# Kernel optimization log

Measured on AMD Instinct MI355X. Metric: run time of the kernel, lower is better.

Reference implementation:

```python
import jax, jax.numpy as jnp
import numpy as np

K, D, B = 2048, 50257, 256
N_CLASS = 2

def setup_inputs() -> dict:
    key = jax.random.key(0)
    k1, k2, k3 = jax.random.split(key, 3)
    # strictly positive (probability-like) entries so log() is finite
    queue_anchor = jax.random.uniform(k1, (K, D), dtype=jnp.float32, minval=1e-3, maxval=1.0)
    query = jax.random.uniform(k2, (B, D), dtype=jnp.float32, minval=1e-3, maxval=1.0)
    queue_label = jax.random.randint(k3, (K,), 0, N_CLASS, dtype=jnp.int64)
    return {"query": query, "queue_anchor": queue_anchor, "queue_label": queue_label}

def reference(query, queue_anchor, queue_label):
    # torch code: mean_d( a[:,None,:] * (log a[:,None,:] - log q) ).T  -> [B, K]
    # algebraically identical, avoiding the (K,B,D) intermediate:
    #   kl[b,k] = mean_d(a_k * log a_k) - (1/D) * sum_d a_k[d] * log q_b[d]
    d = queue_anchor.shape[1]
    self_term = jnp.mean(queue_anchor * jnp.log(queue_anchor), axis=1)        # [K]
    cross_term = jnp.einsum('kd,bd->kb', queue_anchor, jnp.log(query)) / d    # [K, B]
    kl_distance = (self_term[:, None] - cross_term).T                          # [B, K]
    # knn == 1 path: nearest anchor's label per query
    return queue_label[jnp.argmin(kl_distance, axis=1)]                        # [B]
```

## Files before the change

### kernel.cpp

```cpp
#include <hip/hip_runtime.h>


constexpr int K    = 2048;
constexpr int D    = 50257;
constexpr int B    = 256;
constexpr int BM   = 32;
constexpr int BK   = 64;
constexpr int DSPL = 25344;
constexpr int LQS  = 25408;
constexpr int NC   = 8;
constexpr float MARGIN = 4.0f;

typedef __attribute__((ext_vector_type(8))) short bf16x8;
typedef __attribute__((ext_vector_type(4))) float f32x4;
typedef __attribute__((ext_vector_type(8))) unsigned short u16x8;

__device__ inline unsigned short f2bf_rne(float f) {
    union { float f; unsigned u; } v; v.f = f;
    unsigned r = v.u + 0x7FFFu + ((v.u >> 16) & 1u);
    return (unsigned short)(r >> 16);
}

__global__ __launch_bounds__(256)
void lq_kernel(const float* __restrict__ q, unsigned short* __restrict__ lq,
               int aoff, int DL)
{
    const int stride = gridDim.x * blockDim.x;
    const int total  = B * (LQS / 8);
    for (int c = blockIdx.x * blockDim.x + threadIdx.x; c < total; c += stride) {
        const int b  = c / (LQS / 8);
        const int o8 = (c % (LQS / 8)) * 8;
        u16x8 w;
#pragma unroll
        for (int j = 0; j < 8; ++j) {
            const int d = o8 + j;
            const float v = (d < DL) ? q[(size_t)b * D + aoff + d] : 1.f;
            w[j] = f2bf_rne(__logf(v));
        }
        *reinterpret_cast<u16x8*>(&lq[(size_t)b * LQS + o8]) = w;
    }
}

__global__ __launch_bounds__(512, 2)
void gemm_kernel(const float* __restrict__ anchor,
                 const unsigned short* __restrict__ lq,
                 float* __restrict__ part,
                 float* __restrict__ selfp,
                 int dc, int DL, int aoff, int zoff)
{
    const int nb8 = gridDim.x >> 3;
    const int g   = (blockIdx.x & 7) * nb8 + (blockIdx.x >> 3);
    const int z   = g >> 6;
    const int x   = g & 63;

    const int t    = threadIdx.x;
    const int k0   = x * BM;
    const int d0   = z * dc;
    const int DLr  = (DL + 63) & ~63;
    const int dend = min(d0 + dc, DLr);

    __shared__ __align__(16) unsigned short lds[(BM + B) * 64];

    const int rowA = t >> 4;
    const int cA   = (t & 15) * 4;
    const int ar   = k0 + rowA;
    const int swA  = (rowA & 7) << 3;
    const float* Arow = anchor + (size_t)ar * D + aoff;

    const int rowQ = t >> 1;
    const int hq   = (t & 1) * 32;
    const int swQ  = (rowQ & 7) << 3;
    const unsigned short* LQrow = lq + (size_t)rowQ * LQS;

    const int w    = t >> 6;
    const int lane = t & 63;
    const int wn   = w * 32;
    const int lrow = lane & 15;
    const int kg   = lane >> 4;

    f32x4 acc[2][2];
#pragma unroll
    for (int mt = 0; mt < 2; ++mt)
#pragma unroll
        for (int nt = 0; nt < 2; ++nt)
#pragma unroll
            for (int i = 0; i < 4; ++i) acc[mt][nt][i] = 0.f;

    float selfacc = 0.f;

    float wf[8]; int ph = 0;
    u16x8 qreg[4];

    auto load_step = [&](int dt) {
        const int dbase = dt + cA;
        if (dbase + 8 <= DL) {
            const size_t g0 = (size_t)ar * D + aoff + dbase;
            ph = (int)(g0 & 3);
            const float4* wp = reinterpret_cast<const float4*>(anchor + (g0 - ph));
            const float4 w0 = wp[0], w1 = wp[1];
            wf[0] = w0.x; wf[1] = w0.y; wf[2] = w0.z; wf[3] = w0.w;
            wf[4] = w1.x; wf[5] = w1.y; wf[6] = w1.z; wf[7] = w1.w;
        } else {
            ph = 0;
#pragma unroll
            for (int j = 0; j < 4; ++j) {
                const int d = dbase + j;
                wf[j] = (d < DL) ? Arow[d] : 0.f;
            }
#pragma unroll
            for (int j = 4; j < 8; ++j) wf[j] = 0.f;
        }
        const int qb = dt + hq;
#pragma unroll
        for (int gg = 0; gg < 4; ++gg)
            qreg[gg] = *reinterpret_cast<const u16x8*>(&LQrow[qb + 8 * gg]);
    };

    auto convert_write = [&]() {
        float s5[5], av[4];
#pragma unroll
        for (int j = 0; j < 5; ++j) s5[j] = (ph & 2) ? wf[j + 2] : wf[j];
#pragma unroll
        for (int j = 0; j < 4; ++j) av[j] = (ph & 1) ? s5[j + 1] : s5[j];
        ushort4 abf;
        {
            float a0 = av[0], a1 = av[1], a2 = av[2], a3 = av[3];
            if (a0 > 0.f) selfacc = fmaf(a0, __logf(a0), selfacc);
            if (a1 > 0.f) selfacc = fmaf(a1, __logf(a1), selfacc);
            if (a2 > 0.f) selfacc = fmaf(a2, __logf(a2), selfacc);
            if (a3 > 0.f) selfacc = fmaf(a3, __logf(a3), selfacc);
            abf = ushort4{f2bf_rne(a0), f2bf_rne(a1), f2bf_rne(a2), f2bf_rne(a3)};
        }
        *reinterpret_cast<ushort4*>(&lds[rowA * 64 + (cA ^ swA)]) = abf;
#pragma unroll
        for (int gg = 0; gg < 4; ++gg)
            *reinterpret_cast<u16x8*>(&lds[(BM + rowQ) * 64 + ((hq + 8 * gg) ^ swQ)]) = qreg[gg];
    };

    auto mfma_phase = [&]() {
#pragma unroll
        for (int half = 0; half < 2; ++half) {
            const int dd = half * 32;
            bf16x8 af[2], qf[2];
#pragma unroll
            for (int mt = 0; mt < 2; ++mt) {
                const int r = mt * 16 + lrow;
                const int c = (dd + kg * 8) ^ ((r & 7) << 3);
                af[mt] = *reinterpret_cast<const bf16x8*>(&lds[r * 64 + c]);
            }
#pragma unroll
            for (int nt = 0; nt < 2; ++nt) {
                const int r = wn + nt * 16 + lrow;
                const int c = (dd + kg * 8) ^ ((r & 7) << 3);
                qf[nt] = *reinterpret_cast<const bf16x8*>(&lds[(BM + r) * 64 + c]);
            }
#pragma unroll
            for (int mt = 0; mt < 2; ++mt)
#pragma unroll
                for (int nt = 0; nt < 2; ++nt)
                    acc[mt][nt] = __builtin_amdgcn_mfma_f32_16x16x32_bf16(
                        af[mt], qf[nt], acc[mt][nt], 0, 0, 0);
        }
    };

    if (d0 < dend) {
        load_step(d0);
        for (int dt = d0; dt < dend; dt += BK) {
            convert_write();
            __syncthreads();
            if (dt + BK < dend) load_step(dt + BK);
            mfma_phase();
            __syncthreads();
        }
    }

#pragma unroll
    for (int mt = 0; mt < 2; ++mt)
#pragma unroll
        for (int nt = 0; nt < 2; ++nt) {
            const int kk = k0 + mt * 16 + kg * 4;
            const int bb = wn + nt * 16 + lrow;
            *reinterpret_cast<f32x4*>(&part[((size_t)z * B + bb) * K + kk]) = acc[mt][nt];
        }

    float s = selfacc;
    s += __shfl_xor(s, 1);
    s += __shfl_xor(s, 2);
    s += __shfl_xor(s, 4);
    s += __shfl_xor(s, 8);
    if ((t & 15) == 0) selfp[(size_t)(zoff + z) * K + ar] = s;
}

__global__ __launch_bounds__(256)
void reduce_kernel(const float* __restrict__ part, float* __restrict__ crossA, int pch)
{
    const int i = blockIdx.x * 256 + threadIdx.x;
    const f32x4* p4 = reinterpret_cast<const f32x4*>(part);
    f32x4 s = p4[i];
    for (int z = 1; z < pch; ++z) {
        const f32x4 v = p4[(size_t)z * (B * K / 4) + i];
#pragma unroll
        for (int j = 0; j < 4; ++j) s[j] += v[j];
    }
    reinterpret_cast<f32x4*>(crossA)[i] = s;
}

__global__ __launch_bounds__(256)
void selfsum_kernel(const float* __restrict__ selfp, float* __restrict__ selftot, int rows)
{
    const int k = blockIdx.x * 256 + threadIdx.x;
    float s = 0.f;
    for (int z = 0; z < rows; ++z) s += selfp[(size_t)z * K + k];
    selftot[k] = s;
}

__global__ __launch_bounds__(256)
void topk_kernel(const float* __restrict__ crossA, const float* __restrict__ part,
                 const float* __restrict__ selftot,
                 int* __restrict__ cand, int* __restrict__ need, int pch)
{
    const int b = blockIdx.x, t = threadIdx.x;
    float v[8];
#pragma unroll
    for (int i = 0; i < 8; ++i) {
        const int k = i * 256 + t;
        float cv = crossA[(size_t)b * K + k];
        for (int z = 0; z < pch; ++z) cv += part[((size_t)z * B + b) * K + k];
        v[i] = selftot[k] - cv;
    }
    __shared__ float sv[256];
    __shared__ int   si[256];
    __shared__ float topv[2];
    for (int r = 0; r < NC; ++r) {
        float bv = 3.4e38f; int bk = K;
#pragma unroll
        for (int i = 0; i < 8; ++i) {
            const int k = i * 256 + t;
            if (v[i] < bv) { bv = v[i]; bk = k; }
        }
        sv[t] = bv; si[t] = bk;
        __syncthreads();
        for (int off = 128; off > 0; off >>= 1) {
            if (t < off) {
                if (sv[t + off] < sv[t] || (sv[t + off] == sv[t] && si[t + off] < si[t])) {
                    sv[t] = sv[t + off]; si[t] = si[t + off];
                }
            }
            __syncthreads();
        }
        const int kwin = si[0];
        if ((kwin & 255) == t) v[kwin >> 8] = 3.4e38f;
        if (t == 0) {
            cand[b * NC + r] = kwin;
            if (r < 2) topv[r] = sv[0];
        }
        __syncthreads();
    }
    if (t == 0) need[b] = (topv[1] - topv[0] < MARGIN) ? 1 : 0;
}

__global__ __launch_bounds__(512)
void rescore_kernel(const float* __restrict__ query, const float* __restrict__ anchor,
                    const int* __restrict__ cand, const int* __restrict__ need,
                    double* __restrict__ pp)
{
    const int b = blockIdx.x, h = blockIdx.y, t = threadIdx.x;
    if (!need[b]) return;
    const int dlo = h * 25129;
    const int dhi = min(D, dlo + 25129);
    int ks[NC];
#pragma unroll
    for (int c = 0; c < NC; ++c) ks[c] = cand[b * NC + c];
    const float* qrow = query + (size_t)b * D;

    double a8[NC];
#pragma unroll
    for (int c = 0; c < NC; ++c) a8[c] = 0.0;

    for (int d = dlo + t; d < dhi; d += 512) {
        const double lqv = (double)logf(qrow[d]);
#pragma unroll
        for (int c = 0; c < NC; ++c)
            a8[c] = fma((double)anchor[(size_t)ks[c] * D + d], lqv, a8[c]);
    }

    __shared__ double red[512];
    for (int c = 0; c < NC; ++c) {
        red[t] = a8[c];
        __syncthreads();
        for (int off = 256; off > 0; off >>= 1) {
            if (t < off) red[t] += red[t + off];
            __syncthreads();
        }
        if (t == 0) pp[((size_t)b * 2 + h) * NC + c] = red[0];
        __syncthreads();
    }
}

__global__ __launch_bounds__(256)
void final_kernel(const double* __restrict__ pp, const float* __restrict__ selftot,
                  const int* __restrict__ cand, const int* __restrict__ need,
                  const int* __restrict__ label, int* __restrict__ out)
{
    const int b = threadIdx.x;
    if (!need[b]) { out[b] = label[cand[b * NC]]; return; }
    float best = 3.4e38f; int bk = K;
#pragma unroll
    for (int c = 0; c < NC; ++c) {
        const int k = cand[b * NC + c];
        const double cv = pp[((size_t)b * 2 + 0) * NC + c] + pp[((size_t)b * 2 + 1) * NC + c];
        const float sc = selftot[k] - (float)cv;
        if (sc < best || (sc == best && k < bk)) { best = sc; bk = k; }
    }
    out[b] = label[bk];
}

extern "C" void kernel_launch(void* const* d_in, const int* in_sizes, int n_in,
                              void* d_out, int out_size, void* d_ws, size_t ws_size,
                              hipStream_t stream)
{
    const float* query  = (const float*)d_in[0];
    const float* anchor = (const float*)d_in[1];
    const int*   label  = (const int*)d_in[2];
    int* out = (int*)d_out;

    size_t cur = 0;
    auto alloc = [&](size_t bytes) -> void* {
        cur = (cur + 255) & ~(size_t)255;
        void* p = (char*)d_ws + cur;
        cur += bytes;
        return p;
    };

    unsigned short* lq      = (unsigned short*)alloc((size_t)B * LQS * 2);
    float*          crossA  = (float*)alloc((size_t)B * K * 4);
    float*          selfp   = (float*)alloc((size_t)12 * K * 4);
    float*          selftot = (float*)alloc((size_t)K * 4);
    int*            cand    = (int*)alloc((size_t)B * NC * 4);
    int*            need    = (int*)alloc((size_t)B * 4);
    double*         pp      = (double*)alloc((size_t)B * 2 * NC * 8);
    const size_t fixed_end  = cur;

    int pch = 1;
    for (int s = 6; s >= 1; --s) {
        if (fixed_end + (size_t)s * B * K * 4 + 256 <= ws_size) { pch = s; break; }
    }
    float* part = (float*)alloc((size_t)pch * B * K * 4);

    const int DL1 = DSPL, DL2 = D - DSPL;
    const int dc1 = ((DL1 + pch - 1) / pch + 63) & ~63;
    const int dc2 = ((DL2 + pch - 1) / pch + 63) & ~63;

    lq_kernel<<<2048, 256, 0, stream>>>(query, lq, 0, DL1);
    gemm_kernel<<<64 * pch, 512, 0, stream>>>(anchor, lq, part, selfp, dc1, DL1, 0, 0);
    reduce_kernel<<<B * K / 4 / 256, 256, 0, stream>>>(part, crossA, pch);

    lq_kernel<<<2048, 256, 0, stream>>>(query, lq, DSPL, DL2);
    gemm_kernel<<<64 * pch, 512, 0, stream>>>(anchor, lq, part, selfp, dc2, DL2, DSPL, pch);

    selfsum_kernel<<<K / 256, 256, 0, stream>>>(selfp, selftot, 2 * pch);
    topk_kernel<<<B, 256, 0, stream>>>(crossA, part, selftot, cand, need, pch);
    rescore_kernel<<<dim3(B, 2), 512, 0, stream>>>(query, anchor, cand, need, pp);
    final_kernel<<<1, 256, 0, stream>>>(pp, selftot, cand, need, label, out);
}
```

Baseline: 630.0 us.

## Double-buffer LDS tiles with two-stage register prefetch in GEMM kernel

Replaces the single LDS buffer and two-barrier loop with a ping-pong LDS buffer and two register staging sets, so global loads for step s+2 and the LDS write for step s+1 overlap the MFMA work of step s. Only one lightweight barrier (lgkmcnt wait plus s_barrier) is issued per step. Anchor loading is also remapped so only half the threads load A, each handling 8 elements with three float4 loads and tail masking instead of a scalar fallback branch. The cost is double the LDS use and more registers, which may reduce occupancy under the 2-blocks-per-CU launch bound.

After: 764.0 us. +21.3%, slower.

```diff
diff --git a/kernel.cpp b/kernel.cpp
--- a/kernel.cpp
+++ b/kernel.cpp
@@ -58,14 +58,15 @@
     const int d0   = z * dc;
     const int DLr  = (DL + 63) & ~63;
     const int dend = min(d0 + dc, DLr);
-
-    __shared__ __align__(16) unsigned short lds[(BM + B) * 64];
-
-    const int rowA = t >> 4;
-    const int cA   = (t & 15) * 4;
-    const int ar   = k0 + rowA;
+    const size_t KD = (size_t)K * D;
+
+    __shared__ __align__(16) unsigned short lds[2][(BM + B) * 64];
+
+    const int rowA = t >> 3;
+    const int cA   = (t & 7) * 8;
+    const int ar   = k0 + (rowA & 31);
     const int swA  = (rowA & 7) << 3;
-    const float* Arow = anchor + (size_t)ar * D + aoff;
+    const bool doA = (t < 256);
 
     const int rowQ = t >> 1;
     const int hq   = (t & 1) * 32;
@@ -88,56 +89,54 @@
 
     float selfacc = 0.f;
 
-    float wf[8]; int ph = 0;
-    u16x8 qreg[4];
-
-    auto load_step = [&](int dt) {
-        const int dbase = dt + cA;
-        if (dbase + 8 <= DL) {
-            const size_t g0 = (size_t)ar * D + aoff + dbase;
+    float wfA0[12]; int phA0 = 0, dbA0 = 0; u16x8 q0[4];
+    float wfA1[12]; int phA1 = 0, dbA1 = 0; u16x8 q1[4];
+
+    auto ld4 = [&](size_t fi) -> float4 {
+        if (fi > KD - 4) fi = KD - 4;
+        return *reinterpret_cast<const float4*>(anchor + fi);
+    };
+
+    auto load_step = [&](int dt, float (&wf)[12], int& ph, int& db, u16x8 (&qr)[4]) {
+        if (doA) {
+            db = dt + cA;
+            const size_t g0 = (size_t)ar * D + aoff + db;
             ph = (int)(g0 & 3);
-            const float4* wp = reinterpret_cast<const float4*>(anchor + (g0 - ph));
-            const float4 w0 = wp[0], w1 = wp[1];
-            wf[0] = w0.x; wf[1] = w0.y; wf[2] = w0.z; wf[3] = w0.w;
-            wf[4] = w1.x; wf[5] = w1.y; wf[6] = w1.z; wf[7] = w1.w;
-        } else {
-            ph = 0;
-#pragma unroll
-            for (int j = 0; j < 4; ++j) {
-                const int d = dbase + j;
-                wf[j] = (d < DL) ? Arow[d] : 0.f;
-            }
-#pragma unroll
-            for (int j = 4; j < 8; ++j) wf[j] = 0.f;
+            const size_t b0 = g0 - ph;
+            const float4 v0 = ld4(b0), v1 = ld4(b0 + 4), v2 = ld4(b0 + 8);
+            wf[0] = v0.x; wf[1]  = v0.y; wf[2]  = v0.z; wf[3]  = v0.w;
+            wf[4] = v1.x; wf[5]  = v1.y; wf[6]  = v1.z; wf[7]  = v1.w;
+            wf[8] = v2.x; wf[9]  = v2.y; wf[10] = v2.z; wf[11] = v2.w;
         }
         const int qb = dt + hq;
 #pragma unroll
         for (int gg = 0; gg < 4; ++gg)
-            qreg[gg] = *reinterpret_cast<const u16x8*>(&LQrow[qb + 8 * gg]);
-    };
-
-    auto convert_write = [&]() {
-        float s5[5], av[4];
-#pragma unroll
-        for (int j = 0; j < 5; ++j) s5[j] = (ph & 2) ? wf[j + 2] : wf[j];
-#pragma unroll
-        for (int j = 0; j < 4; ++j) av[j] = (ph & 1) ? s5[j + 1] : s5[j];
-        ushort4 abf;
-        {
-            float a0 = av[0], a1 = av[1], a2 = av[2], a3 = av[3];
-            if (a0 > 0.f) selfacc = fmaf(a0, __logf(a0), selfacc);
-            if (a1 > 0.f) selfacc = fmaf(a1, __logf(a1), selfacc);
-            if (a2 > 0.f) selfacc = fmaf(a2, __logf(a2), selfacc);
-            if (a3 > 0.f) selfacc = fmaf(a3, __logf(a3), selfacc);
-            abf = ushort4{f2bf_rne(a0), f2bf_rne(a1), f2bf_rne(a2), f2bf_rne(a3)};
-        }
-        *reinterpret_cast<ushort4*>(&lds[rowA * 64 + (cA ^ swA)]) = abf;
+            qr[gg] = *reinterpret_cast<const u16x8*>(&LQrow[qb + 8 * gg]);
+    };
+
+    auto convert_write = [&](unsigned short* L, float (&wf)[12], int ph, int db,
+                             u16x8 (&qr)[4]) {
+        if (doA) {
+            float s9[9], av[8];
+#pragma unroll
+            for (int j = 0; j < 9; ++j) s9[j] = (ph & 2) ? wf[j + 2] : wf[j];
+#pragma unroll
+            for (int j = 0; j < 8; ++j) av[j] = (ph & 1) ? s9[j + 1] : s9[j];
+            u16x8 abf;
+#pragma unroll
+            for (int j = 0; j < 8; ++j) {
+                float a = (db + j < DL) ? av[j] : 0.f;
+                if (a > 0.f) selfacc = fmaf(a, __logf(a), selfacc);
+                abf[j] = (short)f2bf_rne(a);
+            }
+            *reinterpret_cast<u16x8*>(&L[rowA * 64 + (cA ^ swA)]) = abf;
+        }
 #pragma unroll
         for (int gg = 0; gg < 4; ++gg)
-            *reinterpret_cast<u16x8*>(&lds[(BM + rowQ) * 64 + ((hq + 8 * gg) ^ swQ)]) = qreg[gg];
-    };
-
-    auto mfma_phase = [&]() {
+            *reinterpret_cast<u16x8*>(&L[(BM + rowQ) * 64 + ((hq + 8 * gg) ^ swQ)]) = qr[gg];
+    };
+
+    auto mfma_phase = [&](const unsigned short* L) {
 #pragma unroll
         for (int half = 0; half < 2; ++half) {
             const int dd = half * 32;
@@ -146,13 +145,13 @@
             for (int mt = 0; mt < 2; ++mt) {
                 const int r = mt * 16 + lrow;
                 const int c = (dd + kg * 8) ^ ((r & 7) << 3);
-                af[mt] = *reinterpret_cast<const bf16x8*>(&lds[r * 64 + c]);
+                af[mt] = *reinterpret_cast<const bf16x8*>(&L[r * 64 + c]);
             }
 #pragma unroll
             for (int nt = 0; nt < 2; ++nt) {
                 const int r = wn + nt * 16 + lrow;
                 const int c = (dd + kg * 8) ^ ((r & 7) << 3);
-                qf[nt] = *reinterpret_cast<const bf16x8*>(&lds[(BM + r) * 64 + c]);
+                qf[nt] = *reinterpret_cast<const bf16x8*>(&L[(BM + r) * 64 + c]);
             }
 #pragma unroll
             for (int mt = 0; mt < 2; ++mt)
@@ -163,14 +162,37 @@
         }
     };
 
+    auto soft_barrier = [&]() {
+        asm volatile("s_waitcnt lgkmcnt(0)" ::: "memory");
+        __builtin_amdgcn_sched_barrier(0);
+        __builtin_amdgcn_s_barrier();
+        __builtin_amdgcn_sched_barrier(0);
+    };
+
     if (d0 < dend) {
-        load_step(d0);
-        for (int dt = d0; dt < dend; dt += BK) {
-            convert_write();
-            __syncthreads();
-            if (dt + BK < dend) load_step(dt + BK);
-            mfma_phase();
-            __syncthreads();
+        const int n = (dend - d0) >> 6;
+        load_step(d0, wfA0, phA0, dbA0, q0);
+        if (n > 1) load_step(d0 + BK, wfA1, phA1, dbA1, q1);
+        convert_write(lds[0], wfA0, phA0, dbA0, q0);
+        soft_barrier();
+        for (int s = 0; s < n; ++s) {
+            if ((s & 1) == 0) {
+                if (s + 2 < n) load_step(d0 + (s + 2) * BK, wfA0, phA0, dbA0, q0);
+                __builtin_amdgcn_sched_barrier(0);
+                mfma_phase(lds[0]);
+                if (s + 1 < n) {
+                    convert_write(lds[1], wfA1, phA1, dbA1, q1);
+                    soft_barrier();
+                }
+            } else {
+                if (s + 2 < n) load_step(d0 + (s + 2) * BK, wfA1, phA1, dbA1, q1);
+                __builtin_amdgcn_sched_barrier(0);
+                mfma_phase(lds[1]);
+                if (s + 1 < n) {
+                    convert_write(lds[0], wfA0, phA0, dbA0, q0);
+                    soft_barrier();
+                }
+            }
         }
     }
 
@@ -187,8 +209,7 @@
     s += __shfl_xor(s, 1);
     s += __shfl_xor(s, 2);
     s += __shfl_xor(s, 4);
-    s += __shfl_xor(s, 8);
-    if ((t & 15) == 0) selfp[(size_t)(zoff + z) * K + ar] = s;
+    if (doA && (t & 7) == 0) selfp[(size_t)(zoff + z) * K + ar] = s;
 }
 
 __global__ __launch_bounds__(256)
```

## Split D across waves with register-resident tiles and LDS reduction in GEMM

Applied to the files above, without the earlier changes.

Rewrites the GEMM kernel so each of 8 waves owns a disjoint slice of D and keeps a 32x256 accumulator tile in registers. Anchor rows are loaded and converted per lane straight into MFMA operands, and log-query fragments are read from a new chunk-major global layout instead of staging through LDS with per-step barriers. Per-wave partial sums are combined at the end through a large LDS reduction. This removes the two barriers per K-step and the LDS staging traffic, at the cost of heavy register pressure, a large LDS footprint that limits occupancy, and a change of split count from up to 6 to powers of two.

Measured after the change: 536.9 us (median of 2 runs). 1.17x faster.

```diff
diff --git a/kernel.cpp b/kernel.cpp
--- a/kernel.cpp
+++ b/kernel.cpp
@@ -4,10 +4,7 @@
 constexpr int K    = 2048;
 constexpr int D    = 50257;
 constexpr int B    = 256;
-constexpr int BM   = 32;
-constexpr int BK   = 64;
 constexpr int DSPL = 25344;
-constexpr int LQS  = 25408;
 constexpr int NC   = 8;
 constexpr float MARGIN = 4.0f;
 
@@ -23,172 +20,187 @@
 
 __global__ __launch_bounds__(256)
 void lq_kernel(const float* __restrict__ q, unsigned short* __restrict__ lq,
-               int aoff, int DL)
+               int aoff, int DL, int nch)
 {
     const int stride = gridDim.x * blockDim.x;
-    const int total  = B * (LQS / 8);
+    const int total  = nch * B * 4;
     for (int c = blockIdx.x * blockDim.x + threadIdx.x; c < total; c += stride) {
-        const int b  = c / (LQS / 8);
-        const int o8 = (c % (LQS / 8)) * 8;
+        const int sub = c & 3;
+        const int b   = (c >> 2) & 255;
+        const int ch  = c >> 10;
+        const int d0  = ch * 32 + sub * 8;
         u16x8 w;
 #pragma unroll
         for (int j = 0; j < 8; ++j) {
-            const int d = o8 + j;
+            const int d = d0 + j;
             const float v = (d < DL) ? q[(size_t)b * D + aoff + d] : 1.f;
             w[j] = f2bf_rne(__logf(v));
         }
-        *reinterpret_cast<u16x8*>(&lq[(size_t)b * LQS + o8]) = w;
-    }
-}
-
-__global__ __launch_bounds__(512, 2)
+        *reinterpret_cast<u16x8*>(&lq[((size_t)ch * B + b) * 32 + sub * 8]) = w;
+    }
+}
+
+__global__ __launch_bounds__(512)
 void gemm_kernel(const float* __restrict__ anchor,
                  const unsigned short* __restrict__ lq,
                  float* __restrict__ part,
                  float* __restrict__ selfp,
-                 int dc, int DL, int aoff, int zoff)
+                 int dc, int DL, int DCAP, int aoff, int zoff)
 {
     const int nb8 = gridDim.x >> 3;
     const int g   = (blockIdx.x & 7) * nb8 + (blockIdx.x >> 3);
     const int z   = g >> 6;
-    const int x   = g & 63;
+    const int kt  = g & 63;
+    const int k0  = kt * 32;
 
     const int t    = threadIdx.x;
-    const int k0   = x * BM;
-    const int d0   = z * dc;
-    const int DLr  = (DL + 63) & ~63;
-    const int dend = min(d0 + dc, DLr);
-
-    __shared__ __align__(16) unsigned short lds[(BM + B) * 64];
-
-    const int rowA = t >> 4;
-    const int cA   = (t & 15) * 4;
-    const int ar   = k0 + rowA;
-    const int swA  = (rowA & 7) << 3;
-    const float* Arow = anchor + (size_t)ar * D + aoff;
-
-    const int rowQ = t >> 1;
-    const int hq   = (t & 1) * 32;
-    const int swQ  = (rowQ & 7) << 3;
-    const unsigned short* LQrow = lq + (size_t)rowQ * LQS;
-
-    const int w    = t >> 6;
+    const int wid  = t >> 6;
     const int lane = t & 63;
-    const int wn   = w * 32;
-    const int lrow = lane & 15;
-    const int kg   = lane >> 4;
-
-    f32x4 acc[2][2];
-#pragma unroll
-    for (int mt = 0; mt < 2; ++mt)
-#pragma unroll
-        for (int nt = 0; nt < 2; ++nt)
-#pragma unroll
-            for (int i = 0; i < 4; ++i) acc[mt][nt][i] = 0.f;
-
-    float selfacc = 0.f;
-
-    float wf[8]; int ph = 0;
-    u16x8 qreg[4];
-
-    auto load_step = [&](int dt) {
-        const int dbase = dt + cA;
-        if (dbase + 8 <= DL) {
-            const size_t g0 = (size_t)ar * D + aoff + dbase;
-            ph = (int)(g0 & 3);
-            const float4* wp = reinterpret_cast<const float4*>(anchor + (g0 - ph));
-            const float4 w0 = wp[0], w1 = wp[1];
-            wf[0] = w0.x; wf[1] = w0.y; wf[2] = w0.z; wf[3] = w0.w;
-            wf[4] = w1.x; wf[5] = w1.y; wf[6] = w1.z; wf[7] = w1.w;
-        } else {
-            ph = 0;
-#pragma unroll
-            for (int j = 0; j < 4; ++j) {
-                const int d = dbase + j;
-                wf[j] = (d < DL) ? Arow[d] : 0.f;
+    const int lr   = lane & 15;
+    const int lg   = lane >> 4;
+
+    const int zd0 = z * dc;
+    const int zd1 = min(zd0 + dc, DCAP);
+    const int wd  = ((dc / 8) + 31) & ~31;
+    const int d0  = zd0 + wid * wd;
+    const int d1  = min(d0 + wd, zd1);
+
+    const size_t KDm4 = (size_t)K * D - 4;
+
+    f32x4 acc0[16], acc1[16];
+#pragma unroll
+    for (int j = 0; j < 16; ++j)
+#pragma unroll
+        for (int i = 0; i < 4; ++i) { acc0[j][i] = 0.f; acc1[j][i] = 0.f; }
+
+    float sacc0 = 0.f, sacc1 = 0.f;
+
+    if (d0 < d1) {
+        const int ar0 = k0 + lr;
+        const int ar1 = ar0 + 16;
+        const size_t gA0 = (size_t)ar0 * D + aoff + d0 + lg * 8;
+        const size_t gA1 = (size_t)ar1 * D + aoff + d0 + lg * 8;
+        const int ph0 = (int)(gA0 & 3);
+        const int ph1 = (int)(gA1 & 3);
+        size_t iA0 = gA0 - ph0;
+        size_t iA1 = gA1 - ph1;
+
+        const unsigned short* qp =
+            lq + ((size_t)(d0 >> 5) * (B * 32) + (size_t)lr * 32 + lg * 8);
+
+        auto ld4 = [&](size_t fi) -> float4 {
+            if (fi > KDm4) fi = KDm4;
+            return *reinterpret_cast<const float4*>(anchor + fi);
+        };
+
+        for (int dd = d0; dd < d1; dd += 32) {
+            const int dbase = dd + lg * 8;
+            bf16x8 af0, af1;
+            {
+                const float4 v0 = ld4(iA0), v1 = ld4(iA0 + 4), v2 = ld4(iA0 + 8);
+                float wf[12] = {v0.x, v0.y, v0.z, v0.w, v1.x, v1.y, v1.z, v1.w,
+                                v2.x, v2.y, v2.z, v2.w};
+                float s9[9];
+#pragma unroll
+                for (int j = 0; j < 9; ++j) s9[j] = (ph0 & 2) ? wf[j + 2] : wf[j];
+#pragma unroll
+                for (int j = 0; j < 8; ++j) {
+                    float a = (ph0 & 1) ? s9[j + 1] : s9[j];
+                    a = (dbase + j < DL) ? a : 0.f;
+                    if (a > 0.f) sacc0 = fmaf(a, __logf(a), sacc0);
+                    af0[j] = (short)f2bf_rne(a);
+                }
+                iA0 += 32;
             }
-#pragma unroll
-            for (int j = 4; j < 8; ++j) wf[j] = 0.f;
-        }
-        const int qb = dt + hq;
-#pragma unroll
-        for (int gg = 0; gg < 4; ++gg)
-            qreg[gg] = *reinterpret_cast<const u16x8*>(&LQrow[qb + 8 * gg]);
-    };
-
-    auto convert_write = [&]() {
-        float s5[5], av[4];
-#pragma unroll
-        for (int j = 0; j < 5; ++j) s5[j] = (ph & 2) ? wf[j + 2] : wf[j];
-#pragma unroll
-        for (int j = 0; j < 4; ++j) av[j] = (ph & 1) ? s5[j + 1] : s5[j];
-        ushort4 abf;
-        {
-            float a0 = av[0], a1 = av[1], a2 = av[2], a3 = av[3];
-            if (a0 > 0.f) selfacc = fmaf(a0, __logf(a0), selfacc);
-            if (a1 > 0.f) selfacc = fmaf(a1, __logf(a1), selfacc);
-            if (a2 > 0.f) selfacc = fmaf(a2, __logf(a2), selfacc);
-            if (a3 > 0.f) selfacc = fmaf(a3, __logf(a3), selfacc);
-            abf = ushort4{f2bf_rne(a0), f2bf_rne(a1), f2bf_rne(a2), f2bf_rne(a3)};
-        }
-        *reinterpret_cast<ushort4*>(&lds[rowA * 64 + (cA ^ swA)]) = abf;
-#pragma unroll
-        for (int gg = 0; gg < 4; ++gg)
-            *reinterpret_cast<u16x8*>(&lds[(BM + rowQ) * 64 + ((hq + 8 * gg) ^ swQ)]) = qreg[gg];
-    };
-
-    auto mfma_phase = [&]() {
-#pragma unroll
-        for (int half = 0; half < 2; ++half) {
-            const int dd = half * 32;
-            bf16x8 af[2], qf[2];
-#pragma unroll
-            for (int mt = 0; mt < 2; ++mt) {
-                const int r = mt * 16 + lrow;
-                const int c = (dd + kg * 8) ^ ((r & 7) << 3);
-                af[mt] = *reinterpret_cast<const bf16x8*>(&lds[r * 64 + c]);
+            {
+                const float4 v0 = ld4(iA1), v1 = ld4(iA1 + 4), v2 = ld4(iA1 + 8);
+                float wf[12] = {v0.x, v0.y, v0.z, v0.w, v1.x, v1.y, v1.z, v1.w,
+                                v2.x, v2.y, v2.z, v2.w};
+                float s9[9];
+#pragma unroll
+                for (int j = 0; j < 9; ++j) s9[j] = (ph1 & 2) ? wf[j + 2] : wf[j];
+#pragma unroll
+                for (int j = 0; j < 8; ++j) {
+                    float a = (ph1 & 1) ? s9[j + 1] : s9[j];
+                    a = (dbase + j < DL) ? a : 0.f;
+                    if (a > 0.f) sacc1 = fmaf(a, __logf(a), sacc1);
+                    af1[j] = (short)f2bf_rne(a);
+                }
+                iA1 += 32;
             }
-#pragma unroll
-            for (int nt = 0; nt < 2; ++nt) {
-                const int r = wn + nt * 16 + lrow;
-                const int c = (dd + kg * 8) ^ ((r & 7) << 3);
-                qf[nt] = *reinterpret_cast<const bf16x8*>(&lds[(BM + r) * 64 + c]);
+            {
+                bf16x8 qf[8];
+#pragma unroll
+                for (int j = 0; j < 8; ++j)
+                    qf[j] = *reinterpret_cast<const bf16x8*>(qp + j * 512);
+#pragma unroll
+                for (int j = 0; j < 8; ++j) {
+                    acc0[j] = __builtin_amdgcn_mfma_f32_16x16x32_bf16(af0, qf[j], acc0[j], 0, 0, 0);
+                    acc1[j] = __builtin_amdgcn_mfma_f32_16x16x32_bf16(af1, qf[j], acc1[j], 0, 0, 0);
+                }
+#pragma unroll
+                for (int j = 0; j < 8; ++j)
+                    qf[j] = *reinterpret_cast<const bf16x8*>(qp + (8 + j) * 512);
+#pragma unroll
+                for (int j = 0; j < 8; ++j) {
+                    acc0[8 + j] = __builtin_amdgcn_mfma_f32_16x16x32_bf16(af0, qf[j], acc0[8 + j], 0, 0, 0);
+                    acc1[8 + j] = __builtin_amdgcn_mfma_f32_16x16x32_bf16(af1, qf[j], acc1[8 + j], 0, 0, 0);
+                }
             }
-#pragma unroll
-            for (int mt = 0; mt < 2; ++mt)
-#pragma unroll
-                for (int nt = 0; nt < 2; ++nt)
-                    acc[mt][nt] = __builtin_amdgcn_mfma_f32_16x16x32_bf16(
-                        af[mt], qf[nt], acc[mt][nt], 0, 0, 0);
-        }
-    };
-
-    if (d0 < dend) {
-        load_step(d0);
-        for (int dt = d0; dt < dend; dt += BK) {
-            convert_write();
-            __syncthreads();
-            if (dt + BK < dend) load_step(dt + BK);
-            mfma_phase();
-            __syncthreads();
-        }
-    }
-
-#pragma unroll
-    for (int mt = 0; mt < 2; ++mt)
-#pragma unroll
-        for (int nt = 0; nt < 2; ++nt) {
-            const int kk = k0 + mt * 16 + kg * 4;
-            const int bb = wn + nt * 16 + lrow;
-            *reinterpret_cast<f32x4*>(&part[((size_t)z * B + bb) * K + kk]) = acc[mt][nt];
-        }
-
-    float s = selfacc;
-    s += __shfl_xor(s, 1);
-    s += __shfl_xor(s, 2);
-    s += __shfl_xor(s, 4);
-    s += __shfl_xor(s, 8);
-    if ((t & 15) == 0) selfp[(size_t)(zoff + z) * K + ar] = s;
+            qp += (size_t)B * 32;
+        }
+    }
+
+    sacc0 += __shfl_xor(sacc0, 16); sacc0 += __shfl_xor(sacc0, 32);
+    sacc1 += __shfl_xor(sacc1, 16); sacc1 += __shfl_xor(sacc1, 32);
+
+    __shared__ __align__(16) float red[4][256 * 36];
+    __shared__ float sred[8][32];
+
+    if (lane < 16) { sred[wid][lr] = sacc0; sred[wid][16 + lr] = sacc1; }
+
+    const int rbase = wid & 3;
+    if (wid < 4) {
+#pragma unroll
+        for (int bt = 0; bt < 16; ++bt) {
+            float* p0 = &red[rbase][(bt * 16 + lr) * 36 + lg * 4];
+            *reinterpret_cast<f32x4*>(p0)      = acc0[bt];
+            *reinterpret_cast<f32x4*>(p0 + 16) = acc1[bt];
+        }
+    }
+    __syncthreads();
+    if (wid >= 4) {
+#pragma unroll
+        for (int bt = 0; bt < 16; ++bt) {
+            float* p0 = &red[rbase][(bt * 16 + lr) * 36 + lg * 4];
+            f32x4 v0 = *reinterpret_cast<f32x4*>(p0);
+            f32x4 v1 = *reinterpret_cast<f32x4*>(p0 + 16);
+#pragma unroll
+            for (int i = 0; i < 4; ++i) { v0[i] += acc0[bt][i]; v1[i] += acc1[bt][i]; }
+            *reinterpret_cast<f32x4*>(p0)      = v0;
+            *reinterpret_cast<f32x4*>(p0 + 16) = v1;
+        }
+    }
+    __syncthreads();
+    for (int i = t; i < 256 * 36; i += 512) {
+        red[0][i] += red[2][i];
+        red[1][i] += red[3][i];
+    }
+    __syncthreads();
+    for (int i = t; i < 256 * 36; i += 512) red[0][i] += red[1][i];
+    if (t < 32) {
+        float s = 0.f;
+#pragma unroll
+        for (int w8 = 0; w8 < 8; ++w8) s += sred[w8][t];
+        selfp[(size_t)(zoff + z) * K + k0 + t] = s;
+    }
+    __syncthreads();
+    for (int i = t; i < 2048; i += 512) {
+        const int b  = i >> 3;
+        const int kq = i & 7;
+        const f32x4 v = *reinterpret_cast<f32x4*>(&red[0][b * 36 + kq * 4]);
+        *reinterpret_cast<f32x4*>(&part[((size_t)z * B + b) * K + k0 + kq * 4]) = v;
+    }
 }
 
 __global__ __launch_bounds__(256)
@@ -324,6 +336,12 @@
     const int*   label  = (const int*)d_in[2];
     int* out = (int*)d_out;
 
+    const int DL1 = DSPL;
+    const int DL2 = D - DSPL;
+    const int nch1 = (DL1 + 31) / 32;
+    const int nch2 = (DL2 + 31) / 32;
+    const int nchmax = nch1;
+
     size_t cur = 0;
     auto alloc = [&](size_t bytes) -> void* {
         cur = (cur + 255) & ~(size_t)255;
@@ -332,7 +350,7 @@
         return p;
     };
 
-    unsigned short* lq      = (unsigned short*)alloc((size_t)B * LQS * 2);
+    unsigned short* lq      = (unsigned short*)alloc((size_t)nchmax * B * 32 * 2);
     float*          crossA  = (float*)alloc((size_t)B * K * 4);
     float*          selfp   = (float*)alloc((size_t)12 * K * 4);
     float*          selftot = (float*)alloc((size_t)K * 4);
@@ -342,21 +360,22 @@
     const size_t fixed_end  = cur;
 
     int pch = 1;
-    for (int s = 6; s >= 1; --s) {
+    for (int s = 4; s >= 1; s >>= 1) {
         if (fixed_end + (size_t)s * B * K * 4 + 256 <= ws_size) { pch = s; break; }
     }
     float* part = (float*)alloc((size_t)pch * B * K * 4);
 
-    const int DL1 = DSPL, DL2 = D - DSPL;
-    const int dc1 = ((DL1 + pch - 1) / pch + 63) & ~63;
-    const int dc2 = ((DL2 + pch - 1) / pch + 63) & ~63;
-
-    lq_kernel<<<2048, 256, 0, stream>>>(query, lq, 0, DL1);
-    gemm_kernel<<<64 * pch, 512, 0, stream>>>(anchor, lq, part, selfp, dc1, DL1, 0, 0);
+    const int dc1 = ((DL1 + pch - 1) / pch + 31) & ~31;
+    const int dc2 = ((DL2 + pch - 1) / pch + 31) & ~31;
+
+    lq_kernel<<<2048, 256, 0, stream>>>(query, lq, 0, DL1, nch1);
+    gemm_kernel<<<64 * pch, 512, 0, stream>>>(anchor, lq, part, selfp,
+                                              dc1, DL1, nch1 * 32, 0, 0);
     reduce_kernel<<<B * K / 4 / 256, 256, 0, stream>>>(part, crossA, pch);
 
-    lq_kernel<<<2048, 256, 0, stream>>>(query, lq, DSPL, DL2);
-    gemm_kernel<<<64 * pch, 512, 0, stream>>>(anchor, lq, part, selfp, dc2, DL2, DSPL, pch);
+    lq_kernel<<<2048, 256, 0, stream>>>(query, lq, DSPL, DL2, nch2);
+    gemm_kernel<<<64 * pch, 512, 0, stream>>>(anchor, lq, part, selfp,
+                                              dc2, DL2, nch2 * 32, DSPL, pch);
 
     selfsum_kernel<<<K / 256, 256, 0, stream>>>(selfp, selftot, 2 * pch);
     topk_kernel<<<B, 256, 0, stream>>>(crossA, part, selftot, cand, need, pch);
```
